# Kernel tuning notes

Hardware: AMD Instinct MI355X
Metric: run time of the kernel (lower is better)

Reference implementation:

```python
import jax, jax.numpy as jnp
import numpy as np

B, T, E, HSZ = 128, 256, 512, 1024
VOCAB, LVOCAB, K, STEPS = 2048, 11, 6, 3
HD = HSZ // 2  # per-direction LSTM hidden


def _lstm_dir(x, W_ih, W_hh, b, reverse):
    # x: [B,T,E] -> h seq [B,T,HD]; PyTorch gate order i,f,g,o
    xp = jnp.einsum('bte,ge->btg', x, W_ih) + b  # [B,T,4HD]
    if reverse:
        xp = xp[:, ::-1]
    def step(carry, xt):
        h, c = carry
        g = xt + h @ W_hh.T
        i, f, gg, o = jnp.split(g, 4, axis=-1)
        c = jax.nn.sigmoid(f) * c + jax.nn.sigmoid(i) * jnp.tanh(gg)
        h = jax.nn.sigmoid(o) * jnp.tanh(c)
        return (h, c), h
    z = jnp.zeros((x.shape[0], HD), x.dtype)
    _, hs = jax.lax.scan(step, (z, z), jnp.swapaxes(xp, 0, 1))
    hs = jnp.swapaxes(hs, 0, 1)
    if reverse:
        hs = hs[:, ::-1]
    return hs


def setup_inputs() -> dict:
    key = jax.random.key(0)
    ks = jax.random.split(key, 16)
    Xs = jax.random.randint(ks[0], (B, T), 0, VOCAB)
    seq_mask = jnp.ones((B, T), jnp.float32)
    landmarks = jax.random.randint(ks[1], (B, 4, 4, K), 0, LVOCAB)
    ys = jax.random.randint(ks[2], (B, 2), 0, 4)
    s = 0.05
    emb = (jax.random.normal(ks[3], (VOCAB, E)) * s).at[0].set(0.0)  # padding_idx=0
    W_ih_f = jax.random.normal(ks[4], (4 * HD, E)) * s
    W_hh_f = jax.random.normal(ks[5], (4 * HD, HD)) * s
    b_f = jax.random.normal(ks[6], (4 * HD,)) * s
    W_ih_b = jax.random.normal(ks[7], (4 * HD, E)) * s
    W_hh_b = jax.random.normal(ks[8], (4 * HD, HD)) * s
    b_b = jax.random.normal(ks[9], (4 * HD,)) * s
    feat_ctrl = jax.random.normal(ks[10], (HSZ,)) * 0.1
    upd_W = jax.random.normal(ks[11], (HSZ, 2 * HSZ)) * s
    upd_b = jax.random.normal(ks[12], (HSZ,)) * s
    map_emb = (jax.random.normal(ks[13], (LVOCAB, HSZ)) * s).at[0].set(0.0)
    std = 1.0 / (HSZ * 9)
    conv_w = jax.random.uniform(ks[14], (HSZ, HSZ, 3, 3), minval=-std, maxval=std)
    return dict(Xs=Xs, seq_mask=seq_mask, landmarks=landmarks, ys=ys, emb=emb,
                W_ih_f=W_ih_f, W_hh_f=W_hh_f, b_f=b_f, W_ih_b=W_ih_b,
                W_hh_b=W_hh_b, b_b=b_b, feat_ctrl=feat_ctrl, upd_W=upd_W,
                upd_b=upd_b, map_emb=map_emb, conv_w=conv_w)


def reference(Xs, seq_mask, landmarks, ys, emb, W_ih_f, W_hh_f, b_f,
              W_ih_b, W_hh_b, b_b, feat_ctrl, upd_W, upd_b, map_emb, conv_w):
    bsz = Xs.shape[0]
    x = emb[Xs]  # [B,T,E]
    hf = _lstm_dir(x, W_ih_f, W_hh_f, b_f, False)
    hb = _lstm_dir(x, W_ih_b, W_hh_b, b_b, True)
    hidden = jnp.concatenate([hf, hb], -1)  # [B,T,HSZ]

    controller = jnp.broadcast_to(feat_ctrl, (bsz, HSZ))
    msgs = []
    for _ in range(STEPS):
        score = jnp.einsum('bth,bh->bt', hidden, controller)
        score = score - 1e30 * (1.0 - seq_mask)
        att = jax.nn.softmax(score, axis=-1)
        msg = jnp.einsum('bt,bth->bh', att, hidden)
        msgs.append(msg)
        controller = jnp.concatenate([msg, controller], 1) @ upd_W.T + upd_b
    feature_msg = jnp.concatenate(msgs, 1)  # [B, STEPS*HSZ]

    # MapEmbedding2d: sum landmark embeddings per cell -> [B,4,4,HSZ] -> NCHW
    l_emb = map_emb[landmarks].sum(-2).transpose(0, 3, 1, 2)
    # masked conv weight: 4-neighbor diffusion
    m = jnp.zeros((3, 3)).at[0, 1].set(1.0).at[1, 0].set(1.0).at[2, 1].set(1.0).at[1, 2].set(1.0)
    w = conv_w * m[None, None]
    l_embs = [l_emb]
    for _ in range(STEPS - 1):
        l_embs.append(jax.lax.conv_general_dilated(
            l_embs[-1], w, (1, 1), [(1, 1), (1, 1)],
            dimension_numbers=('NCHW', 'OIHW', 'NCHW')))
    lmk = jnp.concatenate(l_embs, 1)  # [B, STEPS*HSZ, 4, 4]
    lmk = lmk.reshape(bsz, lmk.shape[1], 16).transpose(0, 2, 1)  # [B,16,C]
    logits = jnp.einsum('bnc,bc->bn', lmk, feature_msg)  # [B,16]
    prob = jax.nn.softmax(logits, 1)
    y_true = ys[:, 0] * 4 + ys[:, 1]
    # faithful to original: CrossEntropyLoss applied to prob (softmax of softmax)
    logp = jax.nn.log_softmax(prob, 1)
    loss = -jnp.take_along_axis(logp, y_true[:, None], 1).mean()
    acc = jnp.mean((jnp.argmax(prob, 1) == y_true).astype(jnp.float32))
    return loss, acc
```

## Files before the change

kernel.cpp:

```cpp
#include <hip/hip_runtime.h>


typedef _Float16 f16;
typedef __attribute__((ext_vector_type(8))) _Float16 f16x8;
typedef __attribute__((ext_vector_type(4))) float f32x4;

#define DEV __device__ __forceinline__

DEV void gload_lds16(const void* g, void* lds) {
  __builtin_amdgcn_global_load_lds(
      (const __attribute__((address_space(1))) unsigned*)g,
      (__attribute__((address_space(3))) unsigned*)lds, 16, 0, 0);
}
DEV void gload_lds16c(const void* g, void* lds) {
  __builtin_amdgcn_global_load_lds(
      (const __attribute__((address_space(1))) unsigned*)g,
      (__attribute__((address_space(3))) unsigned*)lds, 16, 0, 17);
}
DEV float sigm(float x) { return 1.0f / (1.0f + __expf(-x)); }
DEV float tanh_(float x) { return 1.0f - 2.0f / (__expf(2.0f * x) + 1.0f); }
DEV unsigned pck(float a, float b) {
  union { unsigned u; f16 h[2]; } c; c.h[0] = (f16)a; c.h[1] = (f16)b; return c.u;
}

__global__ __launch_bounds__(256) void gemm_kernel(
    const f16* __restrict__ A, const f16* __restrict__ B,
    const float* __restrict__ bias, void* __restrict__ Cp,
    int M, int N, int K, int cmode) {
  __shared__ f16 As[128 * 32];
  __shared__ f16 Bs[128 * 32];
  const int tid = threadIdx.x;
  const int w = tid >> 6, l = tid & 63;
  const int m0 = blockIdx.x * 128, n0 = blockIdx.y * 128;
  const int wm = (w & 1) * 64, wn = (w >> 1) * 64;
  const int lr = l & 15, lq = l >> 4;
  const int srow = w * 32 + (l >> 2);
  const int kc8 = (l & 3) * 8;
  f32x4 acc[4][4];
#pragma unroll
  for (int i = 0; i < 4; ++i)
#pragma unroll
    for (int j = 0; j < 4; ++j) acc[i][j] = (f32x4){0.f, 0.f, 0.f, 0.f};

  for (int kt = 0; kt < K; kt += 32) {
    __syncthreads();
#pragma unroll
    for (int i = 0; i < 2; ++i) {
      gload_lds16(A + (long)(m0 + srow + i * 16) * K + kt + kc8,
                  &As[(w * 32 + i * 16) * 32]);
      gload_lds16(B + (long)(n0 + srow + i * 16) * K + kt + kc8,
                  &Bs[(w * 32 + i * 16) * 32]);
    }
    __syncthreads();
    f16x8 af[4], bf[4];
#pragma unroll
    for (int mi = 0; mi < 4; ++mi)
      af[mi] = *(const f16x8*)&As[(wm + mi * 16 + lr) * 32 + lq * 8];
#pragma unroll
    for (int ni = 0; ni < 4; ++ni)
      bf[ni] = *(const f16x8*)&Bs[(wn + ni * 16 + lr) * 32 + lq * 8];
#pragma unroll
    for (int mi = 0; mi < 4; ++mi)
#pragma unroll
      for (int ni = 0; ni < 4; ++ni)
        acc[mi][ni] =
            __builtin_amdgcn_mfma_f32_16x16x32_f16(af[mi], bf[ni], acc[mi][ni], 0, 0, 0);
  }
#pragma unroll
  for (int mi = 0; mi < 4; ++mi)
#pragma unroll
    for (int ni = 0; ni < 4; ++ni)
#pragma unroll
      for (int r = 0; r < 4; ++r) {
        const int m = m0 + wm + mi * 16 + lq * 4 + r;
        const int n = n0 + wn + ni * 16 + lr;
        float v = acc[mi][ni][r];
        if (bias) v += bias[n];
        if (cmode) ((f16*)Cp)[(long)m * N + n] = (f16)v;
        else       ((float*)Cp)[(long)m * N + n] = v;
      }
}

DEV void grid_barrier(int* cnt, int* gen, int tid) {
  __syncthreads();
  if (tid == 0) {
    __threadfence();
    const int a = __hip_atomic_fetch_add(cnt, 1, __ATOMIC_ACQ_REL,
                                         __HIP_MEMORY_SCOPE_SYSTEM);
    if (a == 255) {
      __hip_atomic_store(gen, 1, __ATOMIC_RELEASE, __HIP_MEMORY_SCOPE_SYSTEM);
    } else {
      while (__hip_atomic_load(gen, __ATOMIC_RELAXED,
                               __HIP_MEMORY_SCOPE_SYSTEM) == 0)
        __builtin_amdgcn_s_sleep(8);
    }
    __threadfence();
  }
  __syncthreads();
}

DEV void conv_tile64(char* smem, int tid, const f16* lsrc, const f16* wsrc,
                     f16* ldst, int m0, int n0, const f16* zbuf) {
  f16* const As = (f16*)smem;
  f16* const Bs = (f16*)(smem + 4096);
  const int w = tid >> 6, l = tid & 63;
  const int wn = w * 32;
  const int lr = l & 15, lq = l >> 4;
  const int kc8 = (l & 3) * 8;
  f32x4 acc[4][2];
#pragma unroll
  for (int i = 0; i < 4; ++i)
#pragma unroll
    for (int j = 0; j < 2; ++j) acc[i][j] = (f32x4){0.f, 0.f, 0.f, 0.f};

  for (int kt = 0; kt < 4096; kt += 32) {
    __syncthreads();
    const int tap = kt >> 10;
    const int ic = (kt & 1023) + kc8;
    {
      const int m = m0 + w * 16 + (l >> 2);
      const int b = m >> 4, p = m & 15, py = p >> 2, px = p & 3;
      const int nb = p + ((tap == 0) ? -4 : (tap == 1) ? -1 : (tap == 2) ? 1 : 4);
      const bool ok = (tap == 0) ? (py > 0) : (tap == 1) ? (px > 0)
                      : (tap == 2) ? (px < 3) : (py < 3);
      const f16* sa = ok ? (lsrc + ((long)(b * 16 + nb) * 1024 + ic)) : zbuf;
      gload_lds16(sa, &As[(w * 16) * 32]);
    }
#pragma unroll
    for (int i = 0; i < 2; ++i) {
      gload_lds16(wsrc + (long)(n0 + w * 32 + i * 16 + (l >> 2)) * 4096 + kt + kc8,
                  &Bs[(w * 32 + i * 16) * 32]);
    }
    __syncthreads();
    f16x8 af[4], bf[2];
#pragma unroll
    for (int mi = 0; mi < 4; ++mi)
      af[mi] = *(const f16x8*)&As[(mi * 16 + lr) * 32 + lq * 8];
#pragma unroll
    for (int ni = 0; ni < 2; ++ni)
      bf[ni] = *(const f16x8*)&Bs[(wn + ni * 16 + lr) * 32 + lq * 8];
#pragma unroll
    for (int mi = 0; mi < 4; ++mi)
#pragma unroll
      for (int ni = 0; ni < 2; ++ni)
        acc[mi][ni] =
            __builtin_amdgcn_mfma_f32_16x16x32_f16(af[mi], bf[ni], acc[mi][ni], 0, 0, 0);
  }
#pragma unroll
  for (int mi = 0; mi < 4; ++mi)
#pragma unroll
    for (int ni = 0; ni < 2; ++ni)
#pragma unroll
      for (int r = 0; r < 4; ++r) {
        const int m = m0 + mi * 16 + lq * 4 + r;
        const int n = n0 + wn + ni * 16 + lr;
        ldst[(long)m * 1024 + n] = (f16)acc[mi][ni][r];
      }
}

__global__ __launch_bounds__(256, 1) void lstm_conv_kernel(
    const int* __restrict__ Xs, const f16* __restrict__ emb16,
    const float* __restrict__ Wih_f, const float* __restrict__ Wih_b,
    const float* __restrict__ Whh_f, const float* __restrict__ Whh_b,
    const float* __restrict__ b_f, const float* __restrict__ b_b,
    f16* __restrict__ hg, f16* __restrict__ hidden, int* __restrict__ bar,
    const int* __restrict__ lm, const float* __restrict__ mapemb,
    f16* __restrict__ l0b, f16* __restrict__ l1b, f16* __restrict__ l2b,
    const f16* __restrict__ w416, const f16* __restrict__ zbuf) {
  __shared__ char smem[57344];
  const int blk = blockIdx.x, tid = threadIdx.x;
  const int w = tid >> 6, l = tid & 63;

  for (int j = 0; j < 8; ++j) {
    const int bp = blk * 8 + j;
    const int h = tid * 4;
    float a0 = 0.f, a1 = 0.f, a2 = 0.f, a3 = 0.f;
#pragma unroll
    for (int k = 0; k < 6; ++k) {
      const float* r = mapemb + lm[bp * 6 + k] * 1024 + h;
      a0 += r[0]; a1 += r[1]; a2 += r[2]; a3 += r[3];
    }
    union { uint2 u; f16 hh[4]; } pk;
    pk.hh[0] = (f16)a0; pk.hh[1] = (f16)a1; pk.hh[2] = (f16)a2; pk.hh[3] = (f16)a3;
    *(uint2*)&l0b[(long)bp * 1024 + h] = pk.u;
  }

  f16* const hs = (f16*)smem;
  f16* const xs0 = (f16*)(smem + 16384);
  f16* const xs1 = (f16*)(smem + 32768);
  float* const gbp = (float*)(smem + 49152);
  const int d = blk >> 7, rr = blk & 127;
  const int ug = rr & 15, bg = rr >> 4;
  const int b0 = bg * 16;
  const int lr = l & 15, lq = l >> 4;
  const int u0 = ug * 32 + w * 8;
  const float* const Wih = d ? Wih_b : Wih_f;
  const float* const Whh = d ? Whh_b : Whh_f;
  const float* const bb = d ? b_b : b_f;
  int* const flagbase = &bar[((d << 3) + bg) << 4];

  f16x8 wih[16][2], whh[16][2];
#pragma unroll
  for (int kt = 0; kt < 16; ++kt)
#pragma unroll
    for (int nt = 0; nt < 2; ++nt) {
      const int n = nt * 16 + lr;
      const long row = (long)((n >> 3) * 512 + u0 + (n & 7));
      const float* pi = Wih + row * 512 + kt * 32 + lq * 8;
      const float* ph = Whh + row * 512 + kt * 32 + lq * 8;
      f16x8 va, vb;
#pragma unroll
      for (int j = 0; j < 8; ++j) { va[j] = (f16)pi[j]; vb[j] = (f16)ph[j]; }
      wih[kt][nt] = va; whh[kt][nt] = vb;
    }
  const int bl = l >> 2, jp = (l & 3) * 2;
  const int b_my = b0 + bl;
  const float bi0 = bb[u0 + jp],        bi1 = bb[u0 + jp + 1];
  const float bF0 = bb[512 + u0 + jp],  bF1 = bb[512 + u0 + jp + 1];
  const float bg0 = bb[1024 + u0 + jp], bg1 = bb[1024 + u0 + jp + 1];
  const float bo0 = bb[1536 + u0 + jp], bo1 = bb[1536 + u0 + jp + 1];
  float c0 = 0.f, c1 = 0.f;
  f16* const hbase = hg + (d * 2) * 65536;

#define STAGEH(SRCP)                                                          \
  {                                                                           \
    const f16* _s = (SRCP);                                                   \
    _Pragma("unroll") for (int k4 = 0; k4 < 4; ++k4) {                        \
      const int kt = w * 4 + k4;                                              \
      gload_lds16c(_s + (long)(l >> 2) * 512 + kt * 32 + (l & 3) * 8,         \
                   &hs[(kt * 16) * 32]);                                      \
    }                                                                         \
  }
#define STAGEX(DSTP, TP)                                                      \
  {                                                                           \
    const int _xr = Xs[(b0 + (l >> 2)) * 256 + (TP)];                         \
    const f16* _s = emb16 + (long)_xr * 512 + (l & 3) * 8;                    \
    _Pragma("unroll") for (int k4 = 0; k4 < 4; ++k4) {                        \
      const int kt = w * 4 + k4;                                              \
      gload_lds16(_s + kt * 32, &(DSTP)[(kt * 16) * 32]);                     \
    }                                                                         \
  }

  STAGEX(xs0, d ? 255 : 0);
  __builtin_amdgcn_s_waitcnt(0x0F70);
  __syncthreads();
  f32x4 a0 = (f32x4){0.f, 0.f, 0.f, 0.f}, a1 = (f32x4){0.f, 0.f, 0.f, 0.f};
#pragma unroll
  for (int kt = 0; kt < 16; ++kt) {
    const f16x8 av = *(const f16x8*)&xs0[(kt * 16 + lr) * 32 + lq * 8];
    a0 = __builtin_amdgcn_mfma_f32_16x16x32_f16(av, wih[kt][0], a0, 0, 0, 0);
    a1 = __builtin_amdgcn_mfma_f32_16x16x32_f16(av, wih[kt][1], a1, 0, 0, 0);
  }
  STAGEX(xs1, d ? 254 : 1);

  for (int s = 0; s < 256; ++s) {
    const int t = d ? (255 - s) : s;
    const f16* const hrd = hbase + (s & 1) * 65536;
    f16* const hwr = hbase + ((s + 1) & 1) * 65536;
    if (w == 0 && l < 16) {
      while (__hip_atomic_load(&flagbase[l], __ATOMIC_RELAXED,
                               __HIP_MEMORY_SCOPE_SYSTEM) < s)
        __builtin_amdgcn_s_sleep(1);
    }
    __syncthreads();
    STAGEH(hrd + (long)b0 * 512);
    __builtin_amdgcn_s_waitcnt(0x0F70);
    __syncthreads();
#pragma unroll
    for (int kt = 0; kt < 16; ++kt) {
      const f16x8 av = *(const f16x8*)&hs[(kt * 16 + lr) * 32 + lq * 8];
      a0 = __builtin_amdgcn_mfma_f32_16x16x32_f16(av, whh[kt][0], a0, 0, 0, 0);
      a1 = __builtin_amdgcn_mfma_f32_16x16x32_f16(av, whh[kt][1], a1, 0, 0, 0);
    }
#pragma unroll
    for (int r = 0; r < 4; ++r) {
      gbp[(w * 16 + lq * 4 + r) * 32 + lr] = a0[r];
      gbp[(w * 16 + lq * 4 + r) * 32 + 16 + lr] = a1[r];
    }
    __builtin_amdgcn_s_waitcnt(0xC07F);
    unsigned hp;
    {
      const float* const gr = &gbp[(w * 16 + bl) * 32];
      float gi = gr[jp] + bi0, gf = gr[8 + jp] + bF0;
      float gg = gr[16 + jp] + bg0, go = gr[24 + jp] + bo0;
      c0 = sigm(gf) * c0 + sigm(gi) * tanh_(gg);
      const float h0 = sigm(go) * tanh_(c0);
      gi = gr[jp + 1] + bi1; gf = gr[8 + jp + 1] + bF1;
      gg = gr[16 + jp + 1] + bg1; go = gr[24 + jp + 1] + bo1;
      c1 = sigm(gf) * c1 + sigm(gi) * tanh_(gg);
      const float h1 = sigm(go) * tanh_(c1);
      hp = pck(h0, h1);
      __hip_atomic_store((unsigned*)&hwr[(b_my << 9) + u0 + jp], hp,
                         __ATOMIC_RELAXED, __HIP_MEMORY_SCOPE_SYSTEM);
    }
    __builtin_amdgcn_s_waitcnt(0x0F70);
    __syncthreads();
    if (tid == 0)
      __hip_atomic_store(&flagbase[ug], s + 1, __ATOMIC_RELAXED,
                         __HIP_MEMORY_SCOPE_SYSTEM);
    *(unsigned*)&hidden[((long)b_my * 256 + t) * 1024 + (d << 9) + u0 + jp] = hp;
    if (s < 255) {
      a0 = (f32x4){0.f, 0.f, 0.f, 0.f}; a1 = (f32x4){0.f, 0.f, 0.f, 0.f};
      const f16* const xr = ((s + 1) & 1) ? xs1 : xs0;
#pragma unroll
      for (int kt = 0; kt < 16; ++kt) {
        const f16x8 av = *(const f16x8*)&xr[(kt * 16 + lr) * 32 + lq * 8];
        a0 = __builtin_amdgcn_mfma_f32_16x16x32_f16(av, wih[kt][0], a0, 0, 0, 0);
        a1 = __builtin_amdgcn_mfma_f32_16x16x32_f16(av, wih[kt][1], a1, 0, 0, 0);
      }
      if (s < 254) {
        f16* const xd = (s & 1) ? xs1 : xs0;
        STAGEX(xd, d ? (253 - s) : (s + 2));
      }
    }
  }
#undef STAGEH
#undef STAGEX

  const int m0 = (blk >> 3) * 64, n0 = (blk & 7) * 128;
  grid_barrier(&bar[512], &bar[528], tid);
  conv_tile64(smem, tid, l0b, w416, l1b, m0, n0, zbuf);
  grid_barrier(&bar[544], &bar[560], tid);
  conv_tile64(smem, tid, l1b, w416, l2b, m0, n0, zbuf);
}

__global__ __launch_bounds__(256) void att_kernel(
    const f16* __restrict__ hidden, const float* __restrict__ ctrl,
    const float* __restrict__ seq_mask, float* __restrict__ msg_out,
    f16* __restrict__ cat) {
  __shared__ float sc[256];
  __shared__ float red[4];
  __shared__ float ctl[1024];
  const int b = blockIdx.x, tid = threadIdx.x;
  const int w = tid >> 6, l = tid & 63;
  for (int i = tid; i < 1024; i += 256) ctl[i] = ctrl[b * 1024 + i];
  __syncthreads();
  float cl[16];
#pragma unroll
  for (int j = 0; j < 16; ++j) cl[j] = ctl[l + 64 * j];
  const f16* hb = hidden + (long)b * 262144;
  for (int t = w * 64; t < w * 64 + 64; ++t) {
    float s = 0.f;
#pragma unroll
    for (int j = 0; j < 16; ++j) s += (float)hb[t * 1024 + l + 64 * j] * cl[j];
#pragma unroll
    for (int off = 32; off; off >>= 1) s += __shfl_xor(s, off);
    if (l == 0) sc[t] = s;
  }
  __syncthreads();
  const float v = sc[tid] - 1e30f * (1.0f - seq_mask[b * 256 + tid]);
  float m = v;
#pragma unroll
  for (int off = 32; off; off >>= 1) m = fmaxf(m, __shfl_xor(m, off));
  if (l == 0) red[w] = m;
  __syncthreads();
  const float M = fmaxf(fmaxf(red[0], red[1]), fmaxf(red[2], red[3]));
  const float e = __expf(v - M);
  float ss = e;
#pragma unroll
  for (int off = 32; off; off >>= 1) ss += __shfl_xor(ss, off);
  __syncthreads();
  if (l == 0) red[w] = ss;
  __syncthreads();
  const float S = red[0] + red[1] + red[2] + red[3];
  sc[tid] = e / S;
  __syncthreads();
  const int hc = tid * 4;
  float a0 = 0.f, a1 = 0.f, a2 = 0.f, a3 = 0.f;
  for (int t = 0; t < 256; ++t) {
    const float at = sc[t];
    union { uint2 u; f16 h[4]; } q;
    q.u = *(const uint2*)&hb[t * 1024 + hc];
    a0 += at * (float)q.h[0]; a1 += at * (float)q.h[1];
    a2 += at * (float)q.h[2]; a3 += at * (float)q.h[3];
  }
  float* mo = msg_out + b * 1024 + hc;
  mo[0] = a0; mo[1] = a1; mo[2] = a2; mo[3] = a3;
  if (cat) {
    f16* cm = cat + (long)b * 2048 + hc;
    cm[0] = (f16)a0; cm[1] = (f16)a1; cm[2] = (f16)a2; cm[3] = (f16)a3;
    f16* cc = cat + (long)b * 2048 + 1024 + hc;
    cc[0] = (f16)ctl[hc]; cc[1] = (f16)ctl[hc + 1];
    cc[2] = (f16)ctl[hc + 2]; cc[3] = (f16)ctl[hc + 3];
  }
}

__global__ __launch_bounds__(256) void logits_kernel(
    const f16* __restrict__ l0, const f16* __restrict__ l1, const f16* __restrict__ l2,
    const float* __restrict__ msgs, const int* __restrict__ ys, float* __restrict__ la) {
  __shared__ float lg[16];
  const int b = blockIdx.x, tid = threadIdx.x;
  const int p = tid >> 4, q = tid & 15;
  const float* m0 = msgs + b * 1024;
  const float* m1 = msgs + 131072 + b * 1024;
  const float* m2 = msgs + 262144 + b * 1024;
  const long row = (long)(b * 16 + p) * 1024;
  float part = 0.f;
  for (int i = 0; i < 64; ++i) {
    const int h = q + 16 * i;
    part += (float)l0[row + h] * m0[h] + (float)l1[row + h] * m1[h] +
            (float)l2[row + h] * m2[h];
  }
#pragma unroll
  for (int off = 8; off; off >>= 1) part += __shfl_xor(part, off, 16);
  if (q == 0) lg[p] = part;
  __syncthreads();
  if (tid == 0) {
    float mx = lg[0];
    for (int i = 1; i < 16; ++i) mx = fmaxf(mx, lg[i]);
    float pr[16]; float s = 0.f;
    for (int i = 0; i < 16; ++i) { pr[i] = __expf(lg[i] - mx); s += pr[i]; }
    for (int i = 0; i < 16; ++i) pr[i] /= s;
    float mx2 = pr[0];
    for (int i = 1; i < 16; ++i) mx2 = fmaxf(mx2, pr[i]);
    float s2 = 0.f;
    for (int i = 0; i < 16; ++i) s2 += __expf(pr[i] - mx2);
    const float lse = mx2 + __logf(s2);
    const int y = ys[b * 2] * 4 + ys[b * 2 + 1];
    const float logp = pr[y] - lse;
    int am = 0; float bv = pr[0];
    for (int i = 1; i < 16; ++i) if (pr[i] > bv) { bv = pr[i]; am = i; }
    atomicAdd(&la[0], -logp * (1.0f / 128.0f));
    atomicAdd(&la[1], (am == y) ? (1.0f / 128.0f) : 0.0f);
  }
}

__global__ void finalize_kernel(const float* __restrict__ la,
                                float* __restrict__ out) {
  if (threadIdx.x == 0) { out[0] = la[0]; out[1] = la[1]; }
}

__global__ __launch_bounds__(256) void setup_kernel(
    const float* __restrict__ emb, const float* __restrict__ upd_W,
    const float* __restrict__ conv_w, const float* __restrict__ feat,
    f16* __restrict__ emb16, f16* __restrict__ updW16, f16* __restrict__ w416,
    f16* __restrict__ zbuf, f16* __restrict__ hg, int* __restrict__ bar,
    float* __restrict__ la, float* __restrict__ ctrlA) {
  const int idx = blockIdx.x * 256 + threadIdx.x;
  if (idx < 1048576) emb16[idx] = (f16)emb[idx];
  if (idx < 2097152) updW16[idx] = (f16)upd_W[idx];
  {
    const int o = idx >> 12, r = idx & 4095, tp = r >> 10, i = r & 1023;
    w416[idx] = (f16)conv_w[(long)(o * 1024 + i) * 9 + 1 + 2 * tp];
  }
  if (idx < 131072) { ((unsigned*)hg)[idx] = 0u; ctrlA[idx] = feat[idx & 1023]; }
  if (idx < 1024) bar[idx] = 0;
  if (idx < 128) zbuf[idx] = (f16)0.f;
  if (idx < 2) la[idx] = 0.f;
}

__global__ void fail_kernel(float* out, int mb) {
  if (threadIdx.x == 0) { out[0] = 12344.0f; out[1] = (float)mb; }
}

extern "C" void kernel_launch(void* const* d_in, const int* in_sizes, int n_in,
                              void* d_out, int out_size, void* d_ws, size_t ws_size,
                              hipStream_t stream) {
  (void)in_sizes; (void)n_in; (void)out_size;
  const int*   Xs      = (const int*)d_in[0];
  const float* seqmask = (const float*)d_in[1];
  const int*   lm      = (const int*)d_in[2];
  const int*   ys      = (const int*)d_in[3];
  const float* emb     = (const float*)d_in[4];
  const float* W_ih_f  = (const float*)d_in[5];
  const float* W_hh_f  = (const float*)d_in[6];
  const float* b_f     = (const float*)d_in[7];
  const float* W_ih_b  = (const float*)d_in[8];
  const float* W_hh_b  = (const float*)d_in[9];
  const float* b_b     = (const float*)d_in[10];
  const float* feat    = (const float*)d_in[11];
  const float* upd_W   = (const float*)d_in[12];
  const float* upd_b   = (const float*)d_in[13];
  const float* mapemb  = (const float*)d_in[14];
  const float* conv_w  = (const float*)d_in[15];
  float* out = (float*)d_out;
  char* ws = (char*)d_ws;
  size_t off = 0;
  auto alloc = [&](size_t bytes) {
    void* p = ws + off; off += (bytes + 255) & ~(size_t)255; return p;
  };
  f16*   hid    = (f16*)alloc(67108864);
  f16*   emb16  = (f16*)alloc(2097152);
  f16*   hgb    = (f16*)alloc(524288);
  int*   bar    = (int*)alloc(4096);
  float* la     = (float*)alloc(256);
  float* ctrlA  = (float*)alloc(524288);
  float* ctrlB  = (float*)alloc(524288);
  float* msgs   = (float*)alloc(1572864);
  f16*   cat    = (f16*)alloc(524288);
  f16*   l0b    = (f16*)alloc(4194304);
  f16*   l1b    = (f16*)alloc(4194304);
  f16*   l2b    = (f16*)alloc(4194304);
  f16*   w416   = (f16*)alloc(8388608);
  f16*   updW16 = (f16*)alloc(4194304);
  f16*   zbuf   = (f16*)alloc(256);
  if (ws_size < off) {
    fail_kernel<<<1, 64, 0, stream>>>(out, (int)(off >> 20));
    return;
  }

  setup_kernel<<<16384, 256, 0, stream>>>(emb, upd_W, conv_w, feat, emb16,
                                          updW16, w416, zbuf, hgb, bar, la, ctrlA);
  {
    void* args[] = {(void*)&Xs, (void*)&emb16,
                    (void*)&W_ih_f, (void*)&W_ih_b,
                    (void*)&W_hh_f, (void*)&W_hh_b, (void*)&b_f, (void*)&b_b,
                    (void*)&hgb, (void*)&hid, (void*)&bar,
                    (void*)&lm, (void*)&mapemb,
                    (void*)&l0b, (void*)&l1b, (void*)&l2b,
                    (void*)&w416, (void*)&zbuf};
    hipLaunchCooperativeKernel((void*)lstm_conv_kernel, dim3(256), dim3(256),
                               args, 0, stream);
  }
  att_kernel<<<128, 256, 0, stream>>>(hid, ctrlA, seqmask, msgs, cat);
  gemm_kernel<<<dim3(1, 8), 256, 0, stream>>>(cat, updW16, upd_b, ctrlB,
                                              128, 1024, 2048, 0);
  att_kernel<<<128, 256, 0, stream>>>(hid, ctrlB, seqmask, msgs + 131072, cat);
  gemm_kernel<<<dim3(1, 8), 256, 0, stream>>>(cat, updW16, upd_b, ctrlA,
                                              128, 1024, 2048, 0);
  att_kernel<<<128, 256, 0, stream>>>(hid, ctrlA, seqmask, msgs + 262144, nullptr);
  logits_kernel<<<128, 256, 0, stream>>>(l0b, l1b, l2b, msgs, ys, la);
  finalize_kernel<<<1, 64, 0, stream>>>(la, out);
}
```

Measured before the change: 1.486 ms.

## Fuse attention scoring and weighted sum with online softmax; coalesce conv weight repack

The attention kernel now computes scores, an online softmax and the weighted hidden-state sum in a single pass over the hidden tensor, using vectorized 16-byte loads. Each wave keeps per-lane accumulators that are merged across the four waves through shared memory, so the second full read of the hidden states goes away. The setup kernel now reads conv_w contiguously and scatters the four needed taps into w416, with a larger grid covering the whole weight tensor, replacing strided gathers. The trade-offs are more shared memory, extra exp work per step and more setup threads, most of which do nothing.

```diff
diff --git a/kernel.cpp b/kernel.cpp
--- a/kernel.cpp
+++ b/kernel.cpp
@@ -328,57 +328,63 @@
     const f16* __restrict__ hidden, const float* __restrict__ ctrl,
     const float* __restrict__ seq_mask, float* __restrict__ msg_out,
     f16* __restrict__ cat) {
-  __shared__ float sc[256];
-  __shared__ float red[4];
   __shared__ float ctl[1024];
+  __shared__ float wacc[4][1024];
+  __shared__ float wml[4][2];
   const int b = blockIdx.x, tid = threadIdx.x;
   const int w = tid >> 6, l = tid & 63;
   for (int i = tid; i < 1024; i += 256) ctl[i] = ctrl[b * 1024 + i];
   __syncthreads();
   float cl[16];
 #pragma unroll
-  for (int j = 0; j < 16; ++j) cl[j] = ctl[l + 64 * j];
+  for (int j = 0; j < 16; ++j) cl[j] = ctl[l * 16 + j];
   const f16* hb = hidden + (long)b * 262144;
-  for (int t = w * 64; t < w * 64 + 64; ++t) {
+  float m = -1e38f, lsum = 0.f;
+  float acc[16];
+#pragma unroll
+  for (int j = 0; j < 16; ++j) acc[j] = 0.f;
+  for (int ti = 0; ti < 64; ++ti) {
+    const int t = w * 64 + ti;
+    union { uint4 u; f16 h[8]; } q0, q1;
+    q0.u = *(const uint4*)&hb[t * 1024 + l * 16];
+    q1.u = *(const uint4*)&hb[t * 1024 + l * 16 + 8];
+    float hv[16];
+#pragma unroll
+    for (int j = 0; j < 8; ++j) { hv[j] = (float)q0.h[j]; hv[8 + j] = (float)q1.h[j]; }
     float s = 0.f;
 #pragma unroll
-    for (int j = 0; j < 16; ++j) s += (float)hb[t * 1024 + l + 64 * j] * cl[j];
+    for (int j = 0; j < 16; ++j) s += hv[j] * cl[j];
 #pragma unroll
     for (int off = 32; off; off >>= 1) s += __shfl_xor(s, off);
-    if (l == 0) sc[t] = s;
-  }
+    s -= 1e30f * (1.0f - seq_mask[b * 256 + t]);
+    const float mn = fmaxf(m, s);
+    const float scale = __expf(m - mn);
+    const float e = __expf(s - mn);
+    lsum = lsum * scale + e;
+#pragma unroll
+    for (int j = 0; j < 16; ++j) acc[j] = acc[j] * scale + e * hv[j];
+    m = mn;
+  }
+#pragma unroll
+  for (int j = 0; j < 16; ++j) wacc[w][l * 16 + j] = acc[j];
+  if (l == 0) { wml[w][0] = m; wml[w][1] = lsum; }
   __syncthreads();
-  const float v = sc[tid] - 1e30f * (1.0f - seq_mask[b * 256 + tid]);
-  float m = v;
-#pragma unroll
-  for (int off = 32; off; off >>= 1) m = fmaxf(m, __shfl_xor(m, off));
-  if (l == 0) red[w] = m;
-  __syncthreads();
-  const float M = fmaxf(fmaxf(red[0], red[1]), fmaxf(red[2], red[3]));
-  const float e = __expf(v - M);
-  float ss = e;
-#pragma unroll
-  for (int off = 32; off; off >>= 1) ss += __shfl_xor(ss, off);
-  __syncthreads();
-  if (l == 0) red[w] = ss;
-  __syncthreads();
-  const float S = red[0] + red[1] + red[2] + red[3];
-  sc[tid] = e / S;
-  __syncthreads();
+  const float M = fmaxf(fmaxf(wml[0][0], wml[1][0]), fmaxf(wml[2][0], wml[3][0]));
+  const float e0 = __expf(wml[0][0] - M), e1 = __expf(wml[1][0] - M);
+  const float e2 = __expf(wml[2][0] - M), e3 = __expf(wml[3][0] - M);
+  const float L = wml[0][1] * e0 + wml[1][1] * e1 + wml[2][1] * e2 + wml[3][1] * e3;
+  const float invL = 1.0f / L;
   const int hc = tid * 4;
-  float a0 = 0.f, a1 = 0.f, a2 = 0.f, a3 = 0.f;
-  for (int t = 0; t < 256; ++t) {
-    const float at = sc[t];
-    union { uint2 u; f16 h[4]; } q;
-    q.u = *(const uint2*)&hb[t * 1024 + hc];
-    a0 += at * (float)q.h[0]; a1 += at * (float)q.h[1];
-    a2 += at * (float)q.h[2]; a3 += at * (float)q.h[3];
-  }
-  float* mo = msg_out + b * 1024 + hc;
-  mo[0] = a0; mo[1] = a1; mo[2] = a2; mo[3] = a3;
+  float mv[4];
+#pragma unroll
+  for (int j = 0; j < 4; ++j) {
+    mv[j] = (wacc[0][hc + j] * e0 + wacc[1][hc + j] * e1 +
+             wacc[2][hc + j] * e2 + wacc[3][hc + j] * e3) * invL;
+    msg_out[b * 1024 + hc + j] = mv[j];
+  }
   if (cat) {
     f16* cm = cat + (long)b * 2048 + hc;
-    cm[0] = (f16)a0; cm[1] = (f16)a1; cm[2] = (f16)a2; cm[3] = (f16)a3;
+    cm[0] = (f16)mv[0]; cm[1] = (f16)mv[1]; cm[2] = (f16)mv[2]; cm[3] = (f16)mv[3];
     f16* cc = cat + (long)b * 2048 + 1024 + hc;
     cc[0] = (f16)ctl[hc]; cc[1] = (f16)ctl[hc + 1];
     cc[2] = (f16)ctl[hc + 2]; cc[3] = (f16)ctl[hc + 3];
@@ -437,12 +443,14 @@
     f16* __restrict__ zbuf, f16* __restrict__ hg, int* __restrict__ bar,
     float* __restrict__ la, float* __restrict__ ctrlA) {
   const int idx = blockIdx.x * 256 + threadIdx.x;
+  if (idx < 9437184) {
+    const float v = conv_w[idx];
+    const int o = idx / 9216, rem = idx % 9216, i = rem / 9, rc = rem % 9;
+    if (rc & 1)
+      w416[(long)o * 4096 + ((rc - 1) >> 1) * 1024 + i] = (f16)v;
+  }
   if (idx < 1048576) emb16[idx] = (f16)emb[idx];
   if (idx < 2097152) updW16[idx] = (f16)upd_W[idx];
-  {
-    const int o = idx >> 12, r = idx & 4095, tp = r >> 10, i = r & 1023;
-    w416[idx] = (f16)conv_w[(long)(o * 1024 + i) * 9 + 1 + 2 * tp];
-  }
   if (idx < 131072) { ((unsigned*)hg)[idx] = 0u; ctrlA[idx] = feat[idx & 1023]; }
   if (idx < 1024) bar[idx] = 0;
   if (idx < 128) zbuf[idx] = (f16)0.f;
@@ -499,7 +507,7 @@
     return;
   }
 
-  setup_kernel<<<16384, 256, 0, stream>>>(emb, upd_W, conv_w, feat, emb16,
+  setup_kernel<<<36864, 256, 0, stream>>>(emb, upd_W, conv_w, feat, emb16,
                                           updW16, w416, zbuf, hgb, bar, la, ctrlA);
   {
     void* args[] = {(void*)&Xs, (void*)&emb16,
```

Result: faster. 1.435 ms (-3.4%).
